# Optimization experiments

Measured on AMD Instinct MI355X. Metric: run time of the kernel, lower is better.

Reference implementation:

```python
import jax, jax.numpy as jnp
import numpy as np

MAX_DEG = 6


def neighbor_lookup(atoms, edges, maskvalue, include_self):
    # atoms: (B, A, F), edges: (B, A, D) with -1 padding
    B, A, F = atoms.shape
    D = edges.shape[-1]
    mask = edges >= 0
    idx = jnp.where(mask, edges, 0).reshape(B, A * D)
    g = jnp.take_along_axis(atoms, idx[:, :, None], axis=1).reshape(B, A, D, F)
    g = jnp.where(mask[..., None], g, maskvalue)
    if include_self:
        g = jnp.concatenate([atoms[:, :, None, :], g], axis=2)  # (B,A,D+1,F)
    return g


def graph_conv(atoms, bonds, edges, W, b):
    # W: (MAX_DEG, F_in+BF, C), b: (MAX_DEG, C)
    deg = (edges >= 0).sum(-1)  # (B, A)
    summed_atoms = neighbor_lookup(atoms, edges, 0.0, True).sum(2)  # self + neighbors
    summed_bonds = bonds.sum(2)
    feats = jnp.concatenate([summed_atoms, summed_bonds], axis=-1)
    out = jnp.zeros(feats.shape[:2] + (W.shape[-1],), feats.dtype)
    for d in range(MAX_DEG):  # small fixed loop over degrees
        h = jax.nn.relu(feats @ W[d] + b[d])
        out = out + jnp.where((deg == d)[..., None], h, 0.0)
    return out


def graph_pool(atoms, edges):
    g = neighbor_lookup(atoms, edges, -jnp.inf, True)  # self included -> finite max
    return g.max(axis=2)


def graph_output(atoms, bonds, edges, Wo, bo):
    deg = (edges >= 0).sum(-1)
    feats = jnp.concatenate([atoms, bonds.sum(2)], axis=-1)
    out = jax.nn.softmax(feats @ Wo + bo, axis=-1)
    mask = (deg != 0)[..., None]  # zero out padded atoms
    return jnp.where(mask, out, 0.0).sum(axis=1)  # (B, hid)


def setup_inputs():
    key = jax.random.key(0)
    ks = jax.random.split(key, 16)
    B, A, D = 4096, 64, 6
    AF, BF, H = 37, 6, 128
    s = lambda k, sh: (jax.random.normal(k, sh, jnp.float32) * 0.05)
    return {
        "atoms": jax.random.normal(ks[0], (B, A, AF), jnp.float32),
        "bonds": jax.random.normal(ks[1], (B, A, D, BF), jnp.float32),
        "edges": jax.random.randint(ks[2], (B, A, D), -1, A),
        "W1": s(ks[3], (MAX_DEG, AF + BF, H)),
        "b1": s(ks[4], (MAX_DEG, H)),
        "W2": s(ks[5], (MAX_DEG, H + BF, H)),
        "b2": s(ks[6], (MAX_DEG, H)),
        "Wo": s(ks[7], (H + BF, H)),
        "bo": s(ks[8], (H,)),
        "Wm1": s(ks[9], (H, H // 2)),
        "bm1": s(ks[10], (H // 2,)),
        "Wm2": s(ks[11], (H // 2, H // 4)),
        "bm2": s(ks[12], (H // 4,)),
        "Wm3": s(ks[13], (H // 4, 1)),
        "bm3": s(ks[14], (1,)),
    }


def reference(atoms, bonds, edges, W1, b1, W2, b2, Wo, bo, Wm1, bm1, Wm2, bm2, Wm3, bm3):
    x = graph_conv(atoms, bonds, edges, W1, b1)
    x = graph_pool(x, edges)
    x = graph_conv(x, bonds, edges, W2, b2)
    x = graph_pool(x, edges)
    fp = graph_output(x, bonds, edges, Wo, bo)
    h = jax.nn.relu(fp @ Wm1 + bm1)
    h = jax.nn.relu(h @ Wm2 + bm2)
    out = (h @ Wm3 + bm3).squeeze()  # (B,)
    return out
```

## Files before the change

kernel.cpp:

```cpp
#include <hip/hip_runtime.h>
#include <math.h>


__device__ __forceinline__ float4 max4(float4 a, float4 b) {
  return make_float4(fmaxf(a.x, b.x), fmaxf(a.y, b.y), fmaxf(a.z, b.z), fmaxf(a.w, b.w));
}

__device__ __forceinline__ float4 nbr_max(const float4* sx4, const int* se, int a, int c4) {
  float4 m = sx4[a * 32 + c4];
#pragma unroll
  for (int d = 0; d < 6; ++d) {
    int e = se[a * 6 + d];
    if (e >= 0) m = max4(m, sx4[e * 32 + c4]);
  }
  return m;
}

__device__ __forceinline__ float4 nbr_sum(const float4* sx4, const int* se, int a, int c4) {
  float4 s = sx4[a * 32 + c4];
#pragma unroll
  for (int d = 0; d < 6; ++d) {
    int e = se[a * 6 + d];
    if (e >= 0) {
      float4 v = sx4[e * 32 + c4];
      s.x += v.x; s.y += v.y; s.z += v.z; s.w += v.w;
    }
  }
  return s;
}

__device__ __forceinline__ float4 nbr_wmax(const float4* sx4, const int* se, const int* sdeg,
                                           int a, int c4) {
  float4 m = make_float4(0.f, 0.f, 0.f, 0.f);
  if (sdeg[a] < 6) m = max4(m, sx4[a * 32 + c4]);
#pragma unroll
  for (int d = 0; d < 6; ++d) {
    int e = se[a * 6 + d];
    if (e >= 0 && sdeg[e] < 6) m = max4(m, sx4[e * 32 + c4]);
  }
  return m;
}

__global__ __launch_bounds__(256, 4) void qsar_fused(
    const float* __restrict__ atoms, const float* __restrict__ bonds,
    const int* __restrict__ edges,
    const float* __restrict__ W1, const float* __restrict__ b1,
    const float* __restrict__ W2, const float* __restrict__ b2,
    const float* __restrict__ Wo, const float* __restrict__ bo,
    const float* __restrict__ Wm1, const float* __restrict__ bm1,
    const float* __restrict__ Wm2, const float* __restrict__ bm2,
    const float* __restrict__ Wm3, const float* __restrict__ bm3,
    float* __restrict__ out)
{
  const int b    = blockIdx.x;
  const int tid  = threadIdx.x;
  const int wid  = tid >> 6;
  const int hid  = tid >> 5;
  const int hl   = tid & 31;

  __shared__ float s_x[64 * 128];
  __shared__ float s_sa[16 * 38];
  __shared__ float s_bsum[64 * 8];
  __shared__ int   s_edges[64 * 6];
  __shared__ int   s_deg[64];
  __shared__ int   s_work[64];
  __shared__ int   s_perm[64];
  __shared__ float s_rsum[64];
  __shared__ int   s_nwork, s_na, s_nz;

  float4* sx4  = reinterpret_cast<float4*>(s_x);
  float*  s_fp = s_sa;
  float*  s_h1 = s_sa + 256;
  float*  s_h2 = s_sa + 320;

  {
    const int* ge = edges + (size_t)b * (64 * 6);
    for (int i = tid; i < 64 * 6; i += 256) s_edges[i] = ge[i];
    const float* gb = bonds + (size_t)b * (64 * 36);
    for (int i = tid; i < 64 * 6; i += 256) {
      int a = i / 6, f = i - a * 6;
      float s = 0.f;
#pragma unroll
      for (int d = 0; d < 6; ++d) s += gb[a * 36 + d * 6 + f];
      s_bsum[a * 8 + f] = s;
    }
#pragma unroll
    for (int j = 0; j < 8; ++j) sx4[tid + j * 256] = make_float4(0.f, 0.f, 0.f, 0.f);
    if (tid == 0) { s_nwork = 0; s_na = 0; s_nz = 0; }
  }
  __syncthreads();

  if (tid < 64) {
    int dcnt = 0;
#pragma unroll
    for (int d = 0; d < 6; ++d) dcnt += (s_edges[tid * 6 + d] >= 0) ? 1 : 0;
    s_deg[tid] = dcnt;
    if (dcnt < 6) { int p = atomicAdd(&s_nwork, 1); s_work[p] = tid; }
  }
  __syncthreads();

  if (tid < 64) {
    int nzf = (s_deg[tid] < 6) ? 1 : 0;
#pragma unroll
    for (int d = 0; d < 6; ++d) {
      int e = s_edges[tid * 6 + d];
      if (e >= 0 && s_deg[e] < 6) nzf = 1;
    }
    if (nzf) { int p = atomicAdd(&s_na, 1); s_perm[p] = tid; }
    else     { int p = atomicAdd(&s_nz, 1); s_perm[63 - p] = tid; }
  }

  {
    const int nw = s_nwork;
    const float* ga = atoms + (size_t)b * (64 * 37);
    const int c0 = hl * 4;
    for (int cb = 0; cb < nw; cb += 16) {
      const int cnt = (nw - cb < 16) ? (nw - cb) : 16;
      for (int i = tid; i < cnt * 37; i += 256) {
        int wi = i / 37, k = i - wi * 37;
        int a = s_work[cb + wi];
        float f = ga[a * 37 + k];
#pragma unroll
        for (int d = 0; d < 6; ++d) {
          int e = s_edges[a * 6 + d];
          if (e >= 0) f += ga[e * 37 + k];
        }
        s_sa[wi * 38 + k] = f;
      }
      __syncthreads();
      for (int w = hid; w < cnt; w += 8) {
        const int a = s_work[cb + w];
        const int d = s_deg[a];
        const float* wp = W1 + d * (43 * 128);
        float4 acc = *reinterpret_cast<const float4*>(&b1[d * 128 + c0]);
#pragma unroll 4
        for (int k = 0; k < 37; ++k) {
          const float f = s_sa[w * 38 + k];
          const float4 w4 = *reinterpret_cast<const float4*>(&wp[k * 128 + c0]);
          acc.x = fmaf(f, w4.x, acc.x); acc.y = fmaf(f, w4.y, acc.y);
          acc.z = fmaf(f, w4.z, acc.z); acc.w = fmaf(f, w4.w, acc.w);
        }
#pragma unroll
        for (int kk = 0; kk < 6; ++kk) {
          const float f = s_bsum[a * 8 + kk];
          const float4 w4 = *reinterpret_cast<const float4*>(&wp[(37 + kk) * 128 + c0]);
          acc.x = fmaf(f, w4.x, acc.x); acc.y = fmaf(f, w4.y, acc.y);
          acc.z = fmaf(f, w4.z, acc.z); acc.w = fmaf(f, w4.w, acc.w);
        }
        *reinterpret_cast<float4*>(&s_x[a * 128 + c0]) =
            make_float4(fmaxf(acc.x, 0.f), fmaxf(acc.y, 0.f),
                        fmaxf(acc.z, 0.f), fmaxf(acc.w, 0.f));
      }
      __syncthreads();
    }
  }
  __syncthreads();

  {
    float4 v0 = nbr_max(sx4, s_edges, (tid + 0 * 256) >> 5, tid & 31);
    float4 v1 = nbr_max(sx4, s_edges, (tid + 1 * 256) >> 5, tid & 31);
    float4 v2 = nbr_max(sx4, s_edges, (tid + 2 * 256) >> 5, tid & 31);
    float4 v3 = nbr_max(sx4, s_edges, (tid + 3 * 256) >> 5, tid & 31);
    float4 v4 = nbr_max(sx4, s_edges, (tid + 4 * 256) >> 5, tid & 31);
    float4 v5 = nbr_max(sx4, s_edges, (tid + 5 * 256) >> 5, tid & 31);
    float4 v6 = nbr_max(sx4, s_edges, (tid + 6 * 256) >> 5, tid & 31);
    float4 v7 = nbr_max(sx4, s_edges, (tid + 7 * 256) >> 5, tid & 31);
    __syncthreads();
    sx4[tid + 0 * 256] = v0; sx4[tid + 1 * 256] = v1;
    sx4[tid + 2 * 256] = v2; sx4[tid + 3 * 256] = v3;
    sx4[tid + 4 * 256] = v4; sx4[tid + 5 * 256] = v5;
    sx4[tid + 6 * 256] = v6; sx4[tid + 7 * 256] = v7;
  }
  __syncthreads();

  {
    const float4 z = make_float4(0.f, 0.f, 0.f, 0.f);
    float4 v0 = z, v1 = z, v2 = z, v3 = z, v4 = z, v5 = z, v6 = z, v7 = z;
    if (s_deg[(tid + 0 * 256) >> 5] < 6) v0 = nbr_sum(sx4, s_edges, (tid + 0 * 256) >> 5, tid & 31);
    if (s_deg[(tid + 1 * 256) >> 5] < 6) v1 = nbr_sum(sx4, s_edges, (tid + 1 * 256) >> 5, tid & 31);
    if (s_deg[(tid + 2 * 256) >> 5] < 6) v2 = nbr_sum(sx4, s_edges, (tid + 2 * 256) >> 5, tid & 31);
    if (s_deg[(tid + 3 * 256) >> 5] < 6) v3 = nbr_sum(sx4, s_edges, (tid + 3 * 256) >> 5, tid & 31);
    if (s_deg[(tid + 4 * 256) >> 5] < 6) v4 = nbr_sum(sx4, s_edges, (tid + 4 * 256) >> 5, tid & 31);
    if (s_deg[(tid + 5 * 256) >> 5] < 6) v5 = nbr_sum(sx4, s_edges, (tid + 5 * 256) >> 5, tid & 31);
    if (s_deg[(tid + 6 * 256) >> 5] < 6) v6 = nbr_sum(sx4, s_edges, (tid + 6 * 256) >> 5, tid & 31);
    if (s_deg[(tid + 7 * 256) >> 5] < 6) v7 = nbr_sum(sx4, s_edges, (tid + 7 * 256) >> 5, tid & 31);
    __syncthreads();
    if (s_deg[(tid + 0 * 256) >> 5] < 6) sx4[tid + 0 * 256] = v0;
    if (s_deg[(tid + 1 * 256) >> 5] < 6) sx4[tid + 1 * 256] = v1;
    if (s_deg[(tid + 2 * 256) >> 5] < 6) sx4[tid + 2 * 256] = v2;
    if (s_deg[(tid + 3 * 256) >> 5] < 6) sx4[tid + 3 * 256] = v3;
    if (s_deg[(tid + 4 * 256) >> 5] < 6) sx4[tid + 4 * 256] = v4;
    if (s_deg[(tid + 5 * 256) >> 5] < 6) sx4[tid + 5 * 256] = v5;
    if (s_deg[(tid + 6 * 256) >> 5] < 6) sx4[tid + 6 * 256] = v6;
    if (s_deg[(tid + 7 * 256) >> 5] < 6) sx4[tid + 7 * 256] = v7;
  }
  __syncthreads();

  {
    const int nw = s_nwork;
    const int c0 = hl * 4;
    for (int w = hid; w < nw; w += 8) {
      const int a = s_work[w];
      const int d = s_deg[a];
      const float* wp = W2 + d * (134 * 128);
      float4 acc = *reinterpret_cast<const float4*>(&b2[d * 128 + c0]);
#pragma unroll 4
      for (int k = 0; k < 128; ++k) {
        const float f = s_x[a * 128 + k];
        const float4 w4 = *reinterpret_cast<const float4*>(&wp[k * 128 + c0]);
        acc.x = fmaf(f, w4.x, acc.x); acc.y = fmaf(f, w4.y, acc.y);
        acc.z = fmaf(f, w4.z, acc.z); acc.w = fmaf(f, w4.w, acc.w);
      }
#pragma unroll
      for (int kk = 0; kk < 6; ++kk) {
        const float f = s_bsum[a * 8 + kk];
        const float4 w4 = *reinterpret_cast<const float4*>(&wp[(128 + kk) * 128 + c0]);
        acc.x = fmaf(f, w4.x, acc.x); acc.y = fmaf(f, w4.y, acc.y);
        acc.z = fmaf(f, w4.z, acc.z); acc.w = fmaf(f, w4.w, acc.w);
      }
      *reinterpret_cast<float4*>(&s_x[a * 128 + c0]) =
          make_float4(fmaxf(acc.x, 0.f), fmaxf(acc.y, 0.f),
                      fmaxf(acc.z, 0.f), fmaxf(acc.w, 0.f));
    }
  }
  __syncthreads();

  {
    float4 v0 = nbr_wmax(sx4, s_edges, s_deg, (tid + 0 * 256) >> 5, tid & 31);
    float4 v1 = nbr_wmax(sx4, s_edges, s_deg, (tid + 1 * 256) >> 5, tid & 31);
    float4 v2 = nbr_wmax(sx4, s_edges, s_deg, (tid + 2 * 256) >> 5, tid & 31);
    float4 v3 = nbr_wmax(sx4, s_edges, s_deg, (tid + 3 * 256) >> 5, tid & 31);
    float4 v4 = nbr_wmax(sx4, s_edges, s_deg, (tid + 4 * 256) >> 5, tid & 31);
    float4 v5 = nbr_wmax(sx4, s_edges, s_deg, (tid + 5 * 256) >> 5, tid & 31);
    float4 v6 = nbr_wmax(sx4, s_edges, s_deg, (tid + 6 * 256) >> 5, tid & 31);
    float4 v7 = nbr_wmax(sx4, s_edges, s_deg, (tid + 7 * 256) >> 5, tid & 31);
    __syncthreads();
    sx4[tid + 0 * 256] = v0; sx4[tid + 1 * 256] = v1;
    sx4[tid + 2 * 256] = v2; sx4[tid + 3 * 256] = v3;
    sx4[tid + 4 * 256] = v4; sx4[tid + 5 * 256] = v5;
    sx4[tid + 6 * 256] = v6; sx4[tid + 7 * 256] = v7;
  }
  __syncthreads();

  {
    const int cg = tid & 31, ag = hid;
    const int c0 = cg * 4;
    const int na = s_na;
    const int nr = (na + 31) >> 5;
    for (int j = 0; j < nr; ++j) {
      const int sl = j * 32 + ag * 4;
      const int at0 = s_perm[sl + 0], at1 = s_perm[sl + 1];
      const int at2 = s_perm[sl + 2], at3 = s_perm[sl + 3];
      float a00 = 0.f, a01 = 0.f, a02 = 0.f, a03 = 0.f;
      float a10 = 0.f, a11 = 0.f, a12 = 0.f, a13 = 0.f;
      float a20 = 0.f, a21 = 0.f, a22 = 0.f, a23 = 0.f;
      float a30 = 0.f, a31 = 0.f, a32 = 0.f, a33 = 0.f;
      if (j * 32 + wid * 8 < na) {
#pragma unroll 4
        for (int k = 0; k < 128; ++k) {
          const float4 w4 = *reinterpret_cast<const float4*>(Wo + k * 128 + c0);
          const float f0 = s_x[at0 * 128 + k], f1 = s_x[at1 * 128 + k];
          const float f2 = s_x[at2 * 128 + k], f3 = s_x[at3 * 128 + k];
          a00 = fmaf(f0, w4.x, a00); a01 = fmaf(f0, w4.y, a01);
          a02 = fmaf(f0, w4.z, a02); a03 = fmaf(f0, w4.w, a03);
          a10 = fmaf(f1, w4.x, a10); a11 = fmaf(f1, w4.y, a11);
          a12 = fmaf(f1, w4.z, a12); a13 = fmaf(f1, w4.w, a13);
          a20 = fmaf(f2, w4.x, a20); a21 = fmaf(f2, w4.y, a21);
          a22 = fmaf(f2, w4.z, a22); a23 = fmaf(f2, w4.w, a23);
          a30 = fmaf(f3, w4.x, a30); a31 = fmaf(f3, w4.y, a31);
          a32 = fmaf(f3, w4.z, a32); a33 = fmaf(f3, w4.w, a33);
        }
#pragma unroll
        for (int kk = 0; kk < 6; ++kk) {
          const float4 w4 = *reinterpret_cast<const float4*>(Wo + (128 + kk) * 128 + c0);
          const float f0 = s_bsum[at0 * 8 + kk], f1 = s_bsum[at1 * 8 + kk];
          const float f2 = s_bsum[at2 * 8 + kk], f3 = s_bsum[at3 * 8 + kk];
          a00 = fmaf(f0, w4.x, a00); a01 = fmaf(f0, w4.y, a01);
          a02 = fmaf(f0, w4.z, a02); a03 = fmaf(f0, w4.w, a03);
          a10 = fmaf(f1, w4.x, a10); a11 = fmaf(f1, w4.y, a11);
          a12 = fmaf(f1, w4.z, a12); a13 = fmaf(f1, w4.w, a13);
          a20 = fmaf(f2, w4.x, a20); a21 = fmaf(f2, w4.y, a21);
          a22 = fmaf(f2, w4.z, a22); a23 = fmaf(f2, w4.w, a23);
          a30 = fmaf(f3, w4.x, a30); a31 = fmaf(f3, w4.y, a31);
          a32 = fmaf(f3, w4.z, a32); a33 = fmaf(f3, w4.w, a33);
        }
      }
      __syncthreads();
      const float4 bo4 = *reinterpret_cast<const float4*>(bo + c0);
      if (sl + 0 < na)
        *reinterpret_cast<float4*>(&s_x[at0 * 128 + c0]) =
            make_float4(a00 + bo4.x, a01 + bo4.y, a02 + bo4.z, a03 + bo4.w);
      if (sl + 1 < na)
        *reinterpret_cast<float4*>(&s_x[at1 * 128 + c0]) =
            make_float4(a10 + bo4.x, a11 + bo4.y, a12 + bo4.z, a13 + bo4.w);
      if (sl + 2 < na)
        *reinterpret_cast<float4*>(&s_x[at2 * 128 + c0]) =
            make_float4(a20 + bo4.x, a21 + bo4.y, a22 + bo4.z, a23 + bo4.w);
      if (sl + 3 < na)
        *reinterpret_cast<float4*>(&s_x[at3 * 128 + c0]) =
            make_float4(a30 + bo4.x, a31 + bo4.y, a32 + bo4.z, a33 + bo4.w);
    }
    const int nz = 64 - na;
    for (int e = tid; e < nz * 128; e += 256) {
      int zi = e >> 7, c = e & 127;
      int a = s_perm[na + zi];
      float acc = bo[c];
#pragma unroll
      for (int kk = 0; kk < 6; ++kk)
        acc = fmaf(s_bsum[a * 8 + kk], Wo[(128 + kk) * 128 + c], acc);
      s_x[a * 128 + c] = acc;
    }
  }
  __syncthreads();

  {
    const int a = tid >> 2, q = tid & 3;
    float* base = &s_x[a * 128 + q * 32];
    const float4 v0 = *reinterpret_cast<const float4*>(base + ((0 + tid) & 7) * 4);
    const float4 v1 = *reinterpret_cast<const float4*>(base + ((1 + tid) & 7) * 4);
    const float4 v2 = *reinterpret_cast<const float4*>(base + ((2 + tid) & 7) * 4);
    const float4 v3 = *reinterpret_cast<const float4*>(base + ((3 + tid) & 7) * 4);
    const float4 v4 = *reinterpret_cast<const float4*>(base + ((4 + tid) & 7) * 4);
    const float4 v5 = *reinterpret_cast<const float4*>(base + ((5 + tid) & 7) * 4);
    const float4 v6 = *reinterpret_cast<const float4*>(base + ((6 + tid) & 7) * 4);
    const float4 v7 = *reinterpret_cast<const float4*>(base + ((7 + tid) & 7) * 4);
    float mx = fmaxf(fmaxf(fmaxf(v0.x, v0.y), fmaxf(v0.z, v0.w)),
                     fmaxf(fmaxf(v1.x, v1.y), fmaxf(v1.z, v1.w)));
    mx = fmaxf(mx, fmaxf(fmaxf(fmaxf(v2.x, v2.y), fmaxf(v2.z, v2.w)),
                         fmaxf(fmaxf(v3.x, v3.y), fmaxf(v3.z, v3.w))));
    mx = fmaxf(mx, fmaxf(fmaxf(fmaxf(v4.x, v4.y), fmaxf(v4.z, v4.w)),
                         fmaxf(fmaxf(v5.x, v5.y), fmaxf(v5.z, v5.w))));
    mx = fmaxf(mx, fmaxf(fmaxf(fmaxf(v6.x, v6.y), fmaxf(v6.z, v6.w)),
                         fmaxf(fmaxf(v7.x, v7.y), fmaxf(v7.z, v7.w))));
    mx = fmaxf(mx, __shfl_xor(mx, 1));
    mx = fmaxf(mx, __shfl_xor(mx, 2));
    float sm = 0.f;
    float4 e0, e1, e2, e3, e4, e5, e6, e7;
    e0.x = __expf(v0.x - mx); e0.y = __expf(v0.y - mx); e0.z = __expf(v0.z - mx); e0.w = __expf(v0.w - mx);
    e1.x = __expf(v1.x - mx); e1.y = __expf(v1.y - mx); e1.z = __expf(v1.z - mx); e1.w = __expf(v1.w - mx);
    e2.x = __expf(v2.x - mx); e2.y = __expf(v2.y - mx); e2.z = __expf(v2.z - mx); e2.w = __expf(v2.w - mx);
    e3.x = __expf(v3.x - mx); e3.y = __expf(v3.y - mx); e3.z = __expf(v3.z - mx); e3.w = __expf(v3.w - mx);
    e4.x = __expf(v4.x - mx); e4.y = __expf(v4.y - mx); e4.z = __expf(v4.z - mx); e4.w = __expf(v4.w - mx);
    e5.x = __expf(v5.x - mx); e5.y = __expf(v5.y - mx); e5.z = __expf(v5.z - mx); e5.w = __expf(v5.w - mx);
    e6.x = __expf(v6.x - mx); e6.y = __expf(v6.y - mx); e6.z = __expf(v6.z - mx); e6.w = __expf(v6.w - mx);
    e7.x = __expf(v7.x - mx); e7.y = __expf(v7.y - mx); e7.z = __expf(v7.z - mx); e7.w = __expf(v7.w - mx);
    sm += e0.x + e0.y + e0.z + e0.w; sm += e1.x + e1.y + e1.z + e1.w;
    sm += e2.x + e2.y + e2.z + e2.w; sm += e3.x + e3.y + e3.z + e3.w;
    sm += e4.x + e4.y + e4.z + e4.w; sm += e5.x + e5.y + e5.z + e5.w;
    sm += e6.x + e6.y + e6.z + e6.w; sm += e7.x + e7.y + e7.z + e7.w;
    *reinterpret_cast<float4*>(base + ((0 + tid) & 7) * 4) = e0;
    *reinterpret_cast<float4*>(base + ((1 + tid) & 7) * 4) = e1;
    *reinterpret_cast<float4*>(base + ((2 + tid) & 7) * 4) = e2;
    *reinterpret_cast<float4*>(base + ((3 + tid) & 7) * 4) = e3;
    *reinterpret_cast<float4*>(base + ((4 + tid) & 7) * 4) = e4;
    *reinterpret_cast<float4*>(base + ((5 + tid) & 7) * 4) = e5;
    *reinterpret_cast<float4*>(base + ((6 + tid) & 7) * 4) = e6;
    *reinterpret_cast<float4*>(base + ((7 + tid) & 7) * 4) = e7;
    sm += __shfl_xor(sm, 1);
    sm += __shfl_xor(sm, 2);
    if (q == 0) s_rsum[a] = (s_deg[a] != 0) ? (1.f / sm) : 0.f;
  }
  __syncthreads();

  {
    const int c = tid & 127, half = tid >> 7;
    float s = 0.f;
    for (int a2 = half * 32; a2 < half * 32 + 32; ++a2)
      s = fmaf(s_x[a2 * 128 + c], s_rsum[a2], s);
    s_fp[half * 128 + c] = s;
  }
  __syncthreads();
  if (tid < 128) s_fp[tid] += s_fp[128 + tid];
  __syncthreads();

  if (tid < 64) {
    float acc = bm1[tid];
    for (int k = 0; k < 128; ++k) acc = fmaf(s_fp[k], Wm1[k * 64 + tid], acc);
    s_h1[tid] = fmaxf(acc, 0.f);
  }
  __syncthreads();
  if (tid < 32) {
    float acc = bm2[tid];
    for (int k = 0; k < 64; ++k) acc = fmaf(s_h1[k], Wm2[k * 32 + tid], acc);
    s_h2[tid] = fmaxf(acc, 0.f);
  }
  __syncthreads();
  if (tid < 64) {
    float p = (tid < 32) ? s_h2[tid] * Wm3[tid] : 0.f;
#pragma unroll
    for (int off = 32; off > 0; off >>= 1) p += __shfl_xor(p, off);
    if (tid == 0) out[b] = p + bm3[0];
  }
}

extern "C" void kernel_launch(void* const* d_in, const int* in_sizes, int n_in,
                              void* d_out, int out_size, void* d_ws, size_t ws_size,
                              hipStream_t stream) {
  const float* atoms = (const float*)d_in[0];
  const float* bonds = (const float*)d_in[1];
  const int*   edges = (const int*)d_in[2];
  const float* W1  = (const float*)d_in[3];
  const float* b1  = (const float*)d_in[4];
  const float* W2  = (const float*)d_in[5];
  const float* b2  = (const float*)d_in[6];
  const float* Wo  = (const float*)d_in[7];
  const float* bo  = (const float*)d_in[8];
  const float* Wm1 = (const float*)d_in[9];
  const float* bm1 = (const float*)d_in[10];
  const float* Wm2 = (const float*)d_in[11];
  const float* bm2 = (const float*)d_in[12];
  const float* Wm3 = (const float*)d_in[13];
  const float* bm3 = (const float*)d_in[14];
  float* out = (float*)d_out;

  const int B = out_size;
  qsar_fused<<<dim3(B), dim3(256), 0, stream>>>(
      atoms, bonds, edges, W1, b1, W2, b2, Wo, bo,
      Wm1, bm1, Wm2, bm2, Wm3, bm3, out);
}
```

Measured before the change: 245.8 us.

## Deduplicate second-pool rows by neighbor mask and restructure output GEMM tiling

Each atom gets a 64-bit mask of the low-degree atoms it depends on. Atoms with identical masks share one representative, so the second pool and the Wo projection run only once per unique mask. The output projection now splits K across four waves with shared-memory atomic reductions over 8-row tiles, and caches the Wo bond tail in shared memory. It also drops the 16-atom chunking of the first conv and splits the head MLP reductions across four threads per output with shuffles. The cost is extra bookkeeping, an O(64^2) scan for duplicates, more shared memory that may lower occupancy, and LDS atomic traffic.

```diff
diff --git a/kernel.cpp b/kernel.cpp
--- a/kernel.cpp
+++ b/kernel.cpp
@@ -1,6 +1,16 @@
 #include <hip/hip_runtime.h>
 #include <math.h>
 
+
+#define ACC16_FMA(W2V) \
+  a0x = fmaf(f0, (W2V).x, a0x); a0y = fmaf(f0, (W2V).y, a0y); \
+  a1x = fmaf(f1, (W2V).x, a1x); a1y = fmaf(f1, (W2V).y, a1y); \
+  a2x = fmaf(f2, (W2V).x, a2x); a2y = fmaf(f2, (W2V).y, a2y); \
+  a3x = fmaf(f3, (W2V).x, a3x); a3y = fmaf(f3, (W2V).y, a3y); \
+  a4x = fmaf(f4, (W2V).x, a4x); a4y = fmaf(f4, (W2V).y, a4y); \
+  a5x = fmaf(f5, (W2V).x, a5x); a5y = fmaf(f5, (W2V).y, a5y); \
+  a6x = fmaf(f6, (W2V).x, a6x); a6y = fmaf(f6, (W2V).y, a6y); \
+  a7x = fmaf(f7, (W2V).x, a7x); a7y = fmaf(f7, (W2V).y, a7y);
 
 __device__ __forceinline__ float4 max4(float4 a, float4 b) {
   return make_float4(fmaxf(a.x, b.x), fmaxf(a.y, b.y), fmaxf(a.z, b.z), fmaxf(a.w, b.w));
@@ -52,23 +62,30 @@
     const float* __restrict__ Wm3, const float* __restrict__ bm3,
     float* __restrict__ out)
 {
-  const int b    = blockIdx.x;
-  const int tid  = threadIdx.x;
-  const int wid  = tid >> 6;
-  const int hid  = tid >> 5;
-  const int hl   = tid & 31;
+  const int b   = blockIdx.x;
+  const int tid = threadIdx.x;
+  const int wv  = tid >> 6;
+  const int ln  = tid & 63;
+  const int hid = tid >> 5;
+  const int hl  = tid & 31;
 
   __shared__ float s_x[64 * 128];
-  __shared__ float s_sa[16 * 38];
+  __shared__ float s_sa[64 * 38];
+  __shared__ float s_wtail[6 * 128];
   __shared__ float s_bsum[64 * 8];
   __shared__ int   s_edges[64 * 6];
+  __shared__ unsigned long long s_mask[64];
   __shared__ int   s_deg[64];
   __shared__ int   s_work[64];
-  __shared__ int   s_perm[64];
+  __shared__ int   s_rep[64];
+  __shared__ int   s_uidx[64];
+  __shared__ int   s_urow[64];
+  __shared__ int   s_uniq[64];
   __shared__ float s_rsum[64];
-  __shared__ int   s_nwork, s_na, s_nz;
+  __shared__ int   s_nwork, s_nu;
 
   float4* sx4  = reinterpret_cast<float4*>(s_x);
+  float*  s_D  = s_sa;
   float*  s_fp = s_sa;
   float*  s_h1 = s_sa + 256;
   float*  s_h2 = s_sa + 320;
@@ -86,7 +103,7 @@
     }
 #pragma unroll
     for (int j = 0; j < 8; ++j) sx4[tid + j * 256] = make_float4(0.f, 0.f, 0.f, 0.f);
-    if (tid == 0) { s_nwork = 0; s_na = 0; s_nz = 0; }
+    if (tid == 0) { s_nwork = 0; s_nu = 0; }
   }
   __syncthreads();
 
@@ -99,64 +116,77 @@
   }
   __syncthreads();
 
-  if (tid < 64) {
-    int nzf = (s_deg[tid] < 6) ? 1 : 0;
-#pragma unroll
-    for (int d = 0; d < 6; ++d) {
-      int e = s_edges[tid * 6 + d];
-      if (e >= 0 && s_deg[e] < 6) nzf = 1;
-    }
-    if (nzf) { int p = atomicAdd(&s_na, 1); s_perm[p] = tid; }
-    else     { int p = atomicAdd(&s_nz, 1); s_perm[63 - p] = tid; }
-  }
-
-  {
+  {
+    if (tid < 64) {
+      unsigned long long m = 0ull;
+      if (s_deg[tid] < 6) m |= 1ull << tid;
+#pragma unroll
+      for (int d = 0; d < 6; ++d) {
+        int e = s_edges[tid * 6 + d];
+        if (e >= 0 && s_deg[e] < 6) m |= 1ull << e;
+      }
+      s_mask[tid] = m;
+    }
     const int nw = s_nwork;
     const float* ga = atoms + (size_t)b * (64 * 37);
+    for (int i = tid; i < nw * 37; i += 256) {
+      int wi = i / 37, k = i - wi * 37;
+      int a = s_work[wi];
+      float f = ga[a * 37 + k];
+#pragma unroll
+      for (int d = 0; d < 6; ++d) {
+        int e = s_edges[a * 6 + d];
+        if (e >= 0) f += ga[e * 37 + k];
+      }
+      s_sa[wi * 38 + k] = f;
+    }
+  }
+  __syncthreads();
+
+  {
+    if (tid < 64) {
+      const unsigned long long m = s_mask[tid];
+      int rep = tid;
+      for (int bb = 0; bb < tid; ++bb)
+        if (s_mask[bb] == m) { rep = bb; break; }
+      s_rep[tid] = rep;
+      if (m != 0ull && rep == tid) {
+        int u = atomicAdd(&s_nu, 1);
+        s_uniq[u] = tid;
+        s_uidx[tid] = u;
+      }
+    }
+    const int nw = s_nwork;
     const int c0 = hl * 4;
-    for (int cb = 0; cb < nw; cb += 16) {
-      const int cnt = (nw - cb < 16) ? (nw - cb) : 16;
-      for (int i = tid; i < cnt * 37; i += 256) {
-        int wi = i / 37, k = i - wi * 37;
-        int a = s_work[cb + wi];
-        float f = ga[a * 37 + k];
-#pragma unroll
-        for (int d = 0; d < 6; ++d) {
-          int e = s_edges[a * 6 + d];
-          if (e >= 0) f += ga[e * 37 + k];
-        }
-        s_sa[wi * 38 + k] = f;
-      }
-      __syncthreads();
-      for (int w = hid; w < cnt; w += 8) {
-        const int a = s_work[cb + w];
-        const int d = s_deg[a];
-        const float* wp = W1 + d * (43 * 128);
-        float4 acc = *reinterpret_cast<const float4*>(&b1[d * 128 + c0]);
+    for (int w = hid; w < nw; w += 8) {
+      const int a = s_work[w];
+      const int d = s_deg[a];
+      const float4* wdf4 = reinterpret_cast<const float4*>(W1 + d * (43 * 128));
+      float4 acc = *reinterpret_cast<const float4*>(&b1[d * 128 + c0]);
 #pragma unroll 4
-        for (int k = 0; k < 37; ++k) {
-          const float f = s_sa[w * 38 + k];
-          const float4 w4 = *reinterpret_cast<const float4*>(&wp[k * 128 + c0]);
-          acc.x = fmaf(f, w4.x, acc.x); acc.y = fmaf(f, w4.y, acc.y);
-          acc.z = fmaf(f, w4.z, acc.z); acc.w = fmaf(f, w4.w, acc.w);
-        }
-#pragma unroll
-        for (int kk = 0; kk < 6; ++kk) {
-          const float f = s_bsum[a * 8 + kk];
-          const float4 w4 = *reinterpret_cast<const float4*>(&wp[(37 + kk) * 128 + c0]);
-          acc.x = fmaf(f, w4.x, acc.x); acc.y = fmaf(f, w4.y, acc.y);
-          acc.z = fmaf(f, w4.z, acc.z); acc.w = fmaf(f, w4.w, acc.w);
-        }
-        *reinterpret_cast<float4*>(&s_x[a * 128 + c0]) =
-            make_float4(fmaxf(acc.x, 0.f), fmaxf(acc.y, 0.f),
-                        fmaxf(acc.z, 0.f), fmaxf(acc.w, 0.f));
-      }
-      __syncthreads();
-    }
-  }
-  __syncthreads();
-
-  {
+      for (int k = 0; k < 37; ++k) {
+        const float ff = s_sa[w * 38 + k];
+        const float4 w4 = wdf4[k * 32 + hl];
+        acc.x = fmaf(ff, w4.x, acc.x); acc.y = fmaf(ff, w4.y, acc.y);
+        acc.z = fmaf(ff, w4.z, acc.z); acc.w = fmaf(ff, w4.w, acc.w);
+      }
+#pragma unroll
+      for (int kk = 0; kk < 6; ++kk) {
+        const float ff = s_bsum[a * 8 + kk];
+        const float4 w4 = wdf4[(37 + kk) * 32 + hl];
+        acc.x = fmaf(ff, w4.x, acc.x); acc.y = fmaf(ff, w4.y, acc.y);
+        acc.z = fmaf(ff, w4.z, acc.z); acc.w = fmaf(ff, w4.w, acc.w);
+      }
+      *reinterpret_cast<float4*>(&s_x[a * 128 + c0]) =
+          make_float4(fmaxf(acc.x, 0.f), fmaxf(acc.y, 0.f),
+                      fmaxf(acc.z, 0.f), fmaxf(acc.w, 0.f));
+    }
+  }
+  __syncthreads();
+
+  {
+    if (tid < 64)
+      s_urow[tid] = (s_mask[tid] != 0ull) ? s_uidx[s_rep[tid]] : -1;
     float4 v0 = nbr_max(sx4, s_edges, (tid + 0 * 256) >> 5, tid & 31);
     float4 v1 = nbr_max(sx4, s_edges, (tid + 1 * 256) >> 5, tid & 31);
     float4 v2 = nbr_max(sx4, s_edges, (tid + 2 * 256) >> 5, tid & 31);
@@ -202,21 +232,21 @@
     for (int w = hid; w < nw; w += 8) {
       const int a = s_work[w];
       const int d = s_deg[a];
-      const float* wp = W2 + d * (134 * 128);
+      const float4* wdf4 = reinterpret_cast<const float4*>(W2 + d * (134 * 128));
       float4 acc = *reinterpret_cast<const float4*>(&b2[d * 128 + c0]);
 #pragma unroll 4
       for (int k = 0; k < 128; ++k) {
-        const float f = s_x[a * 128 + k];
-        const float4 w4 = *reinterpret_cast<const float4*>(&wp[k * 128 + c0]);
-        acc.x = fmaf(f, w4.x, acc.x); acc.y = fmaf(f, w4.y, acc.y);
-        acc.z = fmaf(f, w4.z, acc.z); acc.w = fmaf(f, w4.w, acc.w);
+        const float ff = s_x[a * 128 + k];
+        const float4 w4 = wdf4[k * 32 + hl];
+        acc.x = fmaf(ff, w4.x, acc.x); acc.y = fmaf(ff, w4.y, acc.y);
+        acc.z = fmaf(ff, w4.z, acc.z); acc.w = fmaf(ff, w4.w, acc.w);
       }
 #pragma unroll
       for (int kk = 0; kk < 6; ++kk) {
-        const float f = s_bsum[a * 8 + kk];
-        const float4 w4 = *reinterpret_cast<const float4*>(&wp[(128 + kk) * 128 + c0]);
-        acc.x = fmaf(f, w4.x, acc.x); acc.y = fmaf(f, w4.y, acc.y);
-        acc.z = fmaf(f, w4.z, acc.z); acc.w = fmaf(f, w4.w, acc.w);
+        const float ff = s_bsum[a * 8 + kk];
+        const float4 w4 = wdf4[(128 + kk) * 32 + hl];
+        acc.x = fmaf(ff, w4.x, acc.x); acc.y = fmaf(ff, w4.y, acc.y);
+        acc.z = fmaf(ff, w4.z, acc.z); acc.w = fmaf(ff, w4.w, acc.w);
       }
       *reinterpret_cast<float4*>(&s_x[a * 128 + c0]) =
           make_float4(fmaxf(acc.x, 0.f), fmaxf(acc.y, 0.f),
@@ -226,92 +256,95 @@
   __syncthreads();
 
   {
-    float4 v0 = nbr_wmax(sx4, s_edges, s_deg, (tid + 0 * 256) >> 5, tid & 31);
-    float4 v1 = nbr_wmax(sx4, s_edges, s_deg, (tid + 1 * 256) >> 5, tid & 31);
-    float4 v2 = nbr_wmax(sx4, s_edges, s_deg, (tid + 2 * 256) >> 5, tid & 31);
-    float4 v3 = nbr_wmax(sx4, s_edges, s_deg, (tid + 3 * 256) >> 5, tid & 31);
-    float4 v4 = nbr_wmax(sx4, s_edges, s_deg, (tid + 4 * 256) >> 5, tid & 31);
-    float4 v5 = nbr_wmax(sx4, s_edges, s_deg, (tid + 5 * 256) >> 5, tid & 31);
-    float4 v6 = nbr_wmax(sx4, s_edges, s_deg, (tid + 6 * 256) >> 5, tid & 31);
-    float4 v7 = nbr_wmax(sx4, s_edges, s_deg, (tid + 7 * 256) >> 5, tid & 31);
+    const int lim = s_nu * 32;
+    const float4 z = make_float4(0.f, 0.f, 0.f, 0.f);
+    float4 v0 = z, v1 = z, v2 = z, v3 = z, v4 = z, v5 = z, v6 = z, v7 = z;
+    const int i0 = tid, i1 = tid + 256, i2 = tid + 512, i3 = tid + 768;
+    const int i4 = tid + 1024, i5 = tid + 1280, i6 = tid + 1536, i7 = tid + 1792;
+    if (i0 < lim) v0 = nbr_wmax(sx4, s_edges, s_deg, s_uniq[i0 >> 5], i0 & 31);
+    if (i1 < lim) v1 = nbr_wmax(sx4, s_edges, s_deg, s_uniq[i1 >> 5], i1 & 31);
+    if (i2 < lim) v2 = nbr_wmax(sx4, s_edges, s_deg, s_uniq[i2 >> 5], i2 & 31);
+    if (i3 < lim) v3 = nbr_wmax(sx4, s_edges, s_deg, s_uniq[i3 >> 5], i3 & 31);
+    if (i4 < lim) v4 = nbr_wmax(sx4, s_edges, s_deg, s_uniq[i4 >> 5], i4 & 31);
+    if (i5 < lim) v5 = nbr_wmax(sx4, s_edges, s_deg, s_uniq[i5 >> 5], i5 & 31);
+    if (i6 < lim) v6 = nbr_wmax(sx4, s_edges, s_deg, s_uniq[i6 >> 5], i6 & 31);
+    if (i7 < lim) v7 = nbr_wmax(sx4, s_edges, s_deg, s_uniq[i7 >> 5], i7 & 31);
     __syncthreads();
-    sx4[tid + 0 * 256] = v0; sx4[tid + 1 * 256] = v1;
-    sx4[tid + 2 * 256] = v2; sx4[tid + 3 * 256] = v3;
-    sx4[tid + 4 * 256] = v4; sx4[tid + 5 * 256] = v5;
-    sx4[tid + 6 * 256] = v6; sx4[tid + 7 * 256] = v7;
-  }
-  __syncthreads();
-
-  {
-    const int cg = tid & 31, ag = hid;
-    const int c0 = cg * 4;
-    const int na = s_na;
-    const int nr = (na + 31) >> 5;
-    for (int j = 0; j < nr; ++j) {
-      const int sl = j * 32 + ag * 4;
-      const int at0 = s_perm[sl + 0], at1 = s_perm[sl + 1];
-      const int at2 = s_perm[sl + 2], at3 = s_perm[sl + 3];
-      float a00 = 0.f, a01 = 0.f, a02 = 0.f, a03 = 0.f;
-      float a10 = 0.f, a11 = 0.f, a12 = 0.f, a13 = 0.f;
-      float a20 = 0.f, a21 = 0.f, a22 = 0.f, a23 = 0.f;
-      float a30 = 0.f, a31 = 0.f, a32 = 0.f, a33 = 0.f;
-      if (j * 32 + wid * 8 < na) {
+    if (i0 < lim) sx4[s_uniq[i0 >> 5] * 32 + (i0 & 31)] = v0;
+    if (i1 < lim) sx4[s_uniq[i1 >> 5] * 32 + (i1 & 31)] = v1;
+    if (i2 < lim) sx4[s_uniq[i2 >> 5] * 32 + (i2 & 31)] = v2;
+    if (i3 < lim) sx4[s_uniq[i3 >> 5] * 32 + (i3 & 31)] = v3;
+    if (i4 < lim) sx4[s_uniq[i4 >> 5] * 32 + (i4 & 31)] = v4;
+    if (i5 < lim) sx4[s_uniq[i5 >> 5] * 32 + (i5 & 31)] = v5;
+    if (i6 < lim) sx4[s_uniq[i6 >> 5] * 32 + (i6 & 31)] = v6;
+    if (i7 < lim) sx4[s_uniq[i7 >> 5] * 32 + (i7 & 31)] = v7;
+  }
+  __syncthreads();
+
+  {
+    for (int i = tid; i < 768; i += 256) s_wtail[i] = Wo[128 * 128 + i];
+    const int nu = s_nu;
+    const int ntile = (nu == 0) ? 1 : ((nu + 7) >> 3);
+    const float2* Wof2 = reinterpret_cast<const float2*>(Wo);
+    for (int t = 0; t < ntile; ++t) {
+      for (int i = tid; i < 1024; i += 256) s_D[i] = 0.f;
+      __syncthreads();
+      {
+        const int u0 = t * 8;
+        const int b0 = ((u0 + 0 < nu) ? s_uniq[u0 + 0] : 0) * 128;
+        const int b1r = ((u0 + 1 < nu) ? s_uniq[u0 + 1] : 0) * 128;
+        const int b2r = ((u0 + 2 < nu) ? s_uniq[u0 + 2] : 0) * 128;
+        const int b3 = ((u0 + 3 < nu) ? s_uniq[u0 + 3] : 0) * 128;
+        const int b4 = ((u0 + 4 < nu) ? s_uniq[u0 + 4] : 0) * 128;
+        const int b5 = ((u0 + 5 < nu) ? s_uniq[u0 + 5] : 0) * 128;
+        const int b6 = ((u0 + 6 < nu) ? s_uniq[u0 + 6] : 0) * 128;
+        const int b7 = ((u0 + 7 < nu) ? s_uniq[u0 + 7] : 0) * 128;
+        const float g0 = (u0 + 0 < nu) ? 1.f : 0.f, g1 = (u0 + 1 < nu) ? 1.f : 0.f;
+        const float g2 = (u0 + 2 < nu) ? 1.f : 0.f, g3 = (u0 + 3 < nu) ? 1.f : 0.f;
+        const float g4 = (u0 + 4 < nu) ? 1.f : 0.f, g5 = (u0 + 5 < nu) ? 1.f : 0.f;
+        const float g6 = (u0 + 6 < nu) ? 1.f : 0.f, g7 = (u0 + 7 < nu) ? 1.f : 0.f;
+        const int k0 = wv * 32;
+        float a0x = 0.f, a0y = 0.f, a1x = 0.f, a1y = 0.f;
+        float a2x = 0.f, a2y = 0.f, a3x = 0.f, a3y = 0.f;
+        float a4x = 0.f, a4y = 0.f, a5x = 0.f, a5y = 0.f;
+        float a6x = 0.f, a6y = 0.f, a7x = 0.f, a7y = 0.f;
 #pragma unroll 4
-        for (int k = 0; k < 128; ++k) {
-          const float4 w4 = *reinterpret_cast<const float4*>(Wo + k * 128 + c0);
-          const float f0 = s_x[at0 * 128 + k], f1 = s_x[at1 * 128 + k];
-          const float f2 = s_x[at2 * 128 + k], f3 = s_x[at3 * 128 + k];
-          a00 = fmaf(f0, w4.x, a00); a01 = fmaf(f0, w4.y, a01);
-          a02 = fmaf(f0, w4.z, a02); a03 = fmaf(f0, w4.w, a03);
-          a10 = fmaf(f1, w4.x, a10); a11 = fmaf(f1, w4.y, a11);
-          a12 = fmaf(f1, w4.z, a12); a13 = fmaf(f1, w4.w, a13);
-          a20 = fmaf(f2, w4.x, a20); a21 = fmaf(f2, w4.y, a21);
-          a22 = fmaf(f2, w4.z, a22); a23 = fmaf(f2, w4.w, a23);
-          a30 = fmaf(f3, w4.x, a30); a31 = fmaf(f3, w4.y, a31);
-          a32 = fmaf(f3, w4.z, a32); a33 = fmaf(f3, w4.w, a33);
+        for (int j = 0; j < 32; ++j) {
+          const int k = k0 + j;
+          const float2 w = Wof2[k * 64 + ln];
+          const float f0 = g0 * s_x[b0 + k],  f1 = g1 * s_x[b1r + k];
+          const float f2 = g2 * s_x[b2r + k], f3 = g3 * s_x[b3 + k];
+          const float f4 = g4 * s_x[b4 + k],  f5 = g5 * s_x[b5 + k];
+          const float f6 = g6 * s_x[b6 + k],  f7 = g7 * s_x[b7 + k];
+          ACC16_FMA(w)
         }
-#pragma unroll
-        for (int kk = 0; kk < 6; ++kk) {
-          const float4 w4 = *reinterpret_cast<const float4*>(Wo + (128 + kk) * 128 + c0);
-          const float f0 = s_bsum[at0 * 8 + kk], f1 = s_bsum[at1 * 8 + kk];
-          const float f2 = s_bsum[at2 * 8 + kk], f3 = s_bsum[at3 * 8 + kk];
-          a00 = fmaf(f0, w4.x, a00); a01 = fmaf(f0, w4.y, a01);
-          a02 = fmaf(f0, w4.z, a02); a03 = fmaf(f0, w4.w, a03);
-          a10 = fmaf(f1, w4.x, a10); a11 = fmaf(f1, w4.y, a11);
-          a12 = fmaf(f1, w4.z, a12); a13 = fmaf(f1, w4.w, a13);
-          a20 = fmaf(f2, w4.x, a20); a21 = fmaf(f2, w4.y, a21);
-          a22 = fmaf(f2, w4.z, a22); a23 = fmaf(f2, w4.w, a23);
-          a30 = fmaf(f3, w4.x, a30); a31 = fmaf(f3, w4.y, a31);
-          a32 = fmaf(f3, w4.z, a32); a33 = fmaf(f3, w4.w, a33);
+        const int cc = 2 * ln;
+        atomicAdd(&s_D[0 * 128 + cc], a0x); atomicAdd(&s_D[0 * 128 + cc + 1], a0y);
+        atomicAdd(&s_D[1 * 128 + cc], a1x); atomicAdd(&s_D[1 * 128 + cc + 1], a1y);
+        atomicAdd(&s_D[2 * 128 + cc], a2x); atomicAdd(&s_D[2 * 128 + cc + 1], a2y);
+        atomicAdd(&s_D[3 * 128 + cc], a3x); atomicAdd(&s_D[3 * 128 + cc + 1], a3y);
+        atomicAdd(&s_D[4 * 128 + cc], a4x); atomicAdd(&s_D[4 * 128 + cc + 1], a4y);
+        atomicAdd(&s_D[5 * 128 + cc], a5x); atomicAdd(&s_D[5 * 128 + cc + 1], a5y);
+        atomicAdd(&s_D[6 * 128 + cc], a6x); atomicAdd(&s_D[6 * 128 + cc + 1], a6y);
+        atomicAdd(&s_D[7 * 128 + cc], a7x); atomicAdd(&s_D[7 * 128 + cc + 1], a7y);
+      }
+      __syncthreads();
+      for (int e = tid; e < 64 * 128; e += 256) {
+        const int a = e >> 7, c = e & 127;
+        const int ur = s_urow[a];
+        const int ta = (ur < 0) ? 0 : (ur >> 3);
+        if (ta == t) {
+          float acc = bo[c];
+#pragma unroll
+          for (int kk = 0; kk < 6; ++kk)
+            acc = fmaf(s_bsum[a * 8 + kk], s_wtail[kk * 128 + c], acc);
+          if (ur >= 0) acc += s_D[(ur & 7) * 128 + c];
+          s_x[a * 128 + c] = acc;
         }
       }
       __syncthreads();
-      const float4 bo4 = *reinterpret_cast<const float4*>(bo + c0);
-      if (sl + 0 < na)
-        *reinterpret_cast<float4*>(&s_x[at0 * 128 + c0]) =
-            make_float4(a00 + bo4.x, a01 + bo4.y, a02 + bo4.z, a03 + bo4.w);
-      if (sl + 1 < na)
-        *reinterpret_cast<float4*>(&s_x[at1 * 128 + c0]) =
-            make_float4(a10 + bo4.x, a11 + bo4.y, a12 + bo4.z, a13 + bo4.w);
-      if (sl + 2 < na)
-        *reinterpret_cast<float4*>(&s_x[at2 * 128 + c0]) =
-            make_float4(a20 + bo4.x, a21 + bo4.y, a22 + bo4.z, a23 + bo4.w);
-      if (sl + 3 < na)
-        *reinterpret_cast<float4*>(&s_x[at3 * 128 + c0]) =
-            make_float4(a30 + bo4.x, a31 + bo4.y, a32 + bo4.z, a33 + bo4.w);
-    }
-    const int nz = 64 - na;
-    for (int e = tid; e < nz * 128; e += 256) {
-      int zi = e >> 7, c = e & 127;
-      int a = s_perm[na + zi];
-      float acc = bo[c];
-#pragma unroll
-      for (int kk = 0; kk < 6; ++kk)
-        acc = fmaf(s_bsum[a * 8 + kk], Wo[(128 + kk) * 128 + c], acc);
-      s_x[a * 128 + c] = acc;
-    }
-  }
-  __syncthreads();
+    }
+  }
 
   {
     const int a = tid >> 2, q = tid & 3;
@@ -373,16 +406,30 @@
   if (tid < 128) s_fp[tid] += s_fp[128 + tid];
   __syncthreads();
 
-  if (tid < 64) {
-    float acc = bm1[tid];
-    for (int k = 0; k < 128; ++k) acc = fmaf(s_fp[k], Wm1[k * 64 + tid], acc);
-    s_h1[tid] = fmaxf(acc, 0.f);
-  }
-  __syncthreads();
-  if (tid < 32) {
-    float acc = bm2[tid];
-    for (int k = 0; k < 64; ++k) acc = fmaf(s_h1[k], Wm2[k * 32 + tid], acc);
-    s_h2[tid] = fmaxf(acc, 0.f);
+  {
+    const int o = tid >> 2, ks = tid & 3;
+    float acc = 0.f;
+#pragma unroll 8
+    for (int tt = 0; tt < 32; ++tt) {
+      const int k = ks * 32 + tt;
+      acc = fmaf(s_fp[k], Wm1[k * 64 + o], acc);
+    }
+    acc += __shfl_xor(acc, 1);
+    acc += __shfl_xor(acc, 2);
+    if (ks == 0) s_h1[o] = fmaxf(acc + bm1[o], 0.f);
+  }
+  __syncthreads();
+  if (tid < 128) {
+    const int o = tid >> 2, ks = tid & 3;
+    float acc = 0.f;
+#pragma unroll
+    for (int tt = 0; tt < 16; ++tt) {
+      const int k = ks * 16 + tt;
+      acc = fmaf(s_h1[k], Wm2[k * 32 + o], acc);
+    }
+    acc += __shfl_xor(acc, 1);
+    acc += __shfl_xor(acc, 2);
+    if (ks == 0) s_h2[o] = fmaxf(acc + bm2[o], 0.f);
   }
   __syncthreads();
   if (tid < 64) {
```

New measurement: 499.6 us. 2.03x slower.
